# Performance work log

Hardware: AMD Instinct MI355X
Metric: run time of the kernel (lower is better)

Reference implementation:

```python
import jax, jax.numpy as jnp
import numpy as np

H = 1024      # hidden_size
I = 4096      # intermediate_size (4*H SwiGLU)
E = 8         # num_experts
TOPK = 2      # num_experts_per_tok


def setup_inputs() -> dict:
    key = jax.random.key(0)
    ks = jax.random.split(key, 6)
    B, S = 4, 2048
    hidden_states = jax.random.normal(ks[0], (B, S, H), dtype=jnp.float32)
    # router gate (no bias)
    gate_w = jax.random.normal(ks[1], (H, E), dtype=jnp.float32) * (1.0 / np.sqrt(H))
    # per-expert SwiGLU weights (xavier-ish scale)
    W1 = jax.random.normal(ks[2], (E, H, I), dtype=jnp.float32) * np.sqrt(2.0 / (H + I))
    W3 = jax.random.normal(ks[3], (E, H, I), dtype=jnp.float32) * np.sqrt(2.0 / (H + I))
    W2 = jax.random.normal(ks[4], (E, I, H), dtype=jnp.float32) * np.sqrt(2.0 / (H + I))
    # per-expert domain embedding (added to expert input), init std 0.02
    dom = jax.random.normal(ks[5], (E, H), dtype=jnp.float32) * 0.02
    return {"hidden_states": hidden_states, "gate_w": gate_w,
            "W1": W1, "W2": W2, "W3": W3, "dom": dom}


def reference(hidden_states, gate_w, W1, W2, W3, dom):
    B, S, Hd = hidden_states.shape
    x = hidden_states.reshape(-1, Hd)                      # [T, H]
    router_logits = x @ gate_w                             # [T, E]
    top_logits, top_idx = jax.lax.top_k(router_logits, TOPK)
    weights = jax.nn.softmax(top_logits, axis=-1)          # [T, K]
    # dense per-(token, expert) combine weight; 0 for unselected experts
    w_dense = jnp.einsum('tk,tke->te', weights,
                         jax.nn.one_hot(top_idx, E, dtype=weights.dtype))  # [T, E]
    out = jnp.zeros_like(x)
    for e in range(E):  # small fixed expert loop (structurally distinct weights)
        xe = x + dom[e]                                    # domain embedding add
        h = jax.nn.silu(xe @ W1[e]) * (xe @ W3[e])         # SwiGLU [T, I]
        out = out + w_dense[:, e:e + 1] * (h @ W2[e])      # weighted combine
    return out.reshape(B, S, Hd)
```

## Files before the change

kernel.cpp:

```cpp
#include <hip/hip_runtime.h>
#include <hip/hip_bf16.h>
#include <stdint.h>

#define T_TOK 8192
#define H_DIM 1024
#define I_DIM 4096
#define NEXP  8
#define BM    128
#define FBK   64
#define RT_TILES 136
#define RMAX (RT_TILES * BM)

typedef __attribute__((ext_vector_type(8))) short bf16x8;
typedef __attribute__((ext_vector_type(4))) float f32x4;

__device__ __forceinline__ unsigned short f2bf(float f) {
    unsigned int u = __float_as_uint(f);
    return (unsigned short)((u + 0x7FFFu + ((u >> 16) & 1u)) >> 16);
}
__device__ __forceinline__ unsigned int pk2(float a, float b) {
    return (unsigned int)f2bf(a) | ((unsigned int)f2bf(b) << 16);
}
__device__ __forceinline__ void gl_lds16(const void* g, void* l) {
    __builtin_amdgcn_global_load_lds(
        (const __attribute__((address_space(1))) unsigned int*)g,
        (__attribute__((address_space(3))) unsigned int*)l, 16, 0, 0);
}

__global__ __launch_bounds__(256) void router_k(const float* __restrict__ x,
                                                const float* __restrict__ gw,
                                                int2* __restrict__ ridx,
                                                float2* __restrict__ rw) {
    __shared__ float gwT[NEXP][H_DIM + 8];
    for (int i = threadIdx.x; i < H_DIM * NEXP; i += 256) {
        const int k = i >> 3, e = i & 7;
        gwT[e][k] = gw[i];
    }
    __syncthreads();
    const int wid = threadIdx.x >> 6, lane = threadIdx.x & 63;
    const int t = blockIdx.x * 4 + wid;
    const float4* xr = (const float4*)(x + (size_t)t * H_DIM);
    float acc[NEXP];
#pragma unroll
    for (int e = 0; e < NEXP; ++e) acc[e] = 0.f;
#pragma unroll
    for (int jj = 0; jj < 4; ++jj) {
        const float4 v = xr[jj * 64 + lane];
        const int kb = jj * 256 + lane * 4;
#pragma unroll
        for (int e = 0; e < NEXP; ++e) {
            const float4 g = *(const float4*)&gwT[e][kb];
            acc[e] += v.x * g.x + v.y * g.y + v.z * g.z + v.w * g.w;
        }
    }
#pragma unroll
    for (int e = 0; e < NEXP; ++e) {
#pragma unroll
        for (int off = 32; off > 0; off >>= 1) acc[e] += __shfl_xor(acc[e], off, 64);
    }
    if (lane == 0) {
        int i0 = 0; float l0 = acc[0];
#pragma unroll
        for (int e = 1; e < NEXP; ++e) if (acc[e] > l0) { l0 = acc[e]; i0 = e; }
        int i1 = -1; float l1 = -3.4e38f;
#pragma unroll
        for (int e = 0; e < NEXP; ++e) if (e != i0 && acc[e] > l1) { l1 = acc[e]; i1 = e; }
        float ee = __expf(l1 - l0);
        float w0 = 1.f / (1.f + ee);
        float w1 = 1.f - w0;
        ridx[t] = make_int2(i0, i1);
        rw[t]   = make_float2(w0, w1);
    }
}

__global__ __launch_bounds__(256) void plan_k(const int2* __restrict__ ridx,
                                              int* __restrict__ offs,
                                              int* __restrict__ rpos) {
    __shared__ int cnt[256][NEXP];
    __shared__ int base_sh[256][NEXP];
    const int tid = threadIdx.x;
    const int t0 = tid * (T_TOK / 256);
    int c[NEXP];
#pragma unroll
    for (int e = 0; e < NEXP; ++e) c[e] = 0;
    for (int j = 0; j < T_TOK / 256; ++j) {
        const int2 ii = ridx[t0 + j];
#pragma unroll
        for (int e = 0; e < NEXP; ++e)
            c[e] += (ii.x == e ? 1 : 0) + (ii.y == e ? 1 : 0);
    }
#pragma unroll
    for (int e = 0; e < NEXP; ++e) cnt[tid][e] = c[e];
    __syncthreads();
    if (tid == 0) {
        int tot[NEXP];
#pragma unroll
        for (int e = 0; e < NEXP; ++e) tot[e] = 0;
        for (int i = 0; i < 256; ++i)
#pragma unroll
            for (int e = 0; e < NEXP; ++e) tot[e] += cnt[i][e];
        int run[NEXP];
        int o = 0;
#pragma unroll
        for (int e = 0; e < NEXP; ++e) {
            offs[e] = o; run[e] = o;
            o += (tot[e] + BM - 1) & ~(BM - 1);
        }
        offs[NEXP] = o;
        for (int i = 0; i < 256; ++i)
#pragma unroll
            for (int e = 0; e < NEXP; ++e) {
                base_sh[i][e] = run[e];
                run[e] += cnt[i][e];
            }
    }
    __syncthreads();
    int b[NEXP];
#pragma unroll
    for (int e = 0; e < NEXP; ++e) b[e] = base_sh[tid][e];
    for (int j = 0; j < T_TOK / 256; ++j) {
        const int2 ii = ridx[t0 + j];
        int r0 = 0, r1 = 0;
#pragma unroll
        for (int e = 0; e < NEXP; ++e) r0 += (ii.x == e ? b[e] : 0);
#pragma unroll
        for (int e = 0; e < NEXP; ++e) b[e] += (ii.x == e ? 1 : 0);
#pragma unroll
        for (int e = 0; e < NEXP; ++e) r1 += (ii.y == e ? b[e] : 0);
#pragma unroll
        for (int e = 0; e < NEXP; ++e) b[e] += (ii.y == e ? 1 : 0);
        rpos[2 * (t0 + j)]     = r0;
        rpos[2 * (t0 + j) + 1] = r1;
    }
}

__global__ __launch_bounds__(256) void scatter_w13t_k(
        const float* __restrict__ x, const float* __restrict__ dom,
        const int2* __restrict__ ridx, const float2* __restrict__ rw,
        const int* __restrict__ rpos, float* __restrict__ rwgt,
        unsigned short* __restrict__ xg,
        const float* __restrict__ W1, const float* __restrict__ W3,
        unsigned short* __restrict__ w13) {
    __shared__ float st[64 * 65];
    if (blockIdx.x < 2048) {
        const int wid = threadIdx.x >> 6, lane = threadIdx.x & 63;
        const int t = blockIdx.x * 4 + wid;
        const int2 ii = ridx[t];
        const float2 ww = rw[t];
        const int r0 = rpos[2 * t], r1 = rpos[2 * t + 1];
        if (lane == 0) {
            rwgt[r0] = ww.x;
            rwgt[r1] = ww.y;
        }
        const float4* xr = (const float4*)(x + (size_t)t * H_DIM);
        float4 xv[4];
#pragma unroll
        for (int jj = 0; jj < 4; ++jj) xv[jj] = xr[jj * 64 + lane];
#pragma unroll
        for (int s = 0; s < 2; ++s) {
            const int e = s ? ii.y : ii.x;
            const int rr = s ? r1 : r0;
            const float4* dr = (const float4*)(dom + (size_t)e * H_DIM);
            unsigned short* op = xg + (size_t)rr * H_DIM;
#pragma unroll
            for (int jj = 0; jj < 4; ++jj) {
                const float4 b = dr[jj * 64 + lane];
                const int kb = jj * 256 + lane * 4;
                *(uint2*)(op + kb) = make_uint2(pk2(xv[jj].x + b.x, xv[jj].y + b.y),
                                                pk2(xv[jj].z + b.z, xv[jj].w + b.w));
            }
        }
    } else {
        const int idx = blockIdx.x - 2048;
        const int nt = idx & 63;
        const int kt = (idx >> 6) & 15;
        const int z  = idx >> 10;
        const int e = z >> 1, sel = z & 1;
        const float* src = (sel ? W3 : W1) + (size_t)e * H_DIM * I_DIM;
        const int t = threadIdx.x;
        const int kr = t >> 2, c0 = (t & 3) << 4;
        const float* sp = src + (size_t)(kt * 64 + kr) * I_DIM + nt * 64 + c0;
#pragma unroll
        for (int j = 0; j < 4; ++j) {
            float4 v = *(const float4*)(sp + j * 4);
            st[kr * 65 + c0 + j*4 + 0] = v.x; st[kr * 65 + c0 + j*4 + 1] = v.y;
            st[kr * 65 + c0 + j*4 + 2] = v.z; st[kr * 65 + c0 + j*4 + 3] = v.w;
        }
        __syncthreads();
        const int nl = t >> 2, k0 = (t & 3) << 4;
        const int n = nt * 64 + nl;
        const size_t drow = (size_t)e * 8192 + (size_t)((n >> 4) << 5) + (sel << 4) + (n & 15);
        unsigned short* dp = w13 + drow * H_DIM + kt * 64 + k0;
        unsigned int pk[8];
#pragma unroll
        for (int j = 0; j < 8; ++j)
            pk[j] = pk2(st[(k0 + 2*j) * 65 + nl], st[(k0 + 2*j + 1) * 65 + nl]);
        *(uint4*)dp = make_uint4(pk[0], pk[1], pk[2], pk[3]);
        *(uint4*)(dp + 8) = make_uint4(pk[4], pk[5], pk[6], pk[7]);
    }
}

__global__ __launch_bounds__(256, 3) void gemm1_w2t_k(
        const unsigned short* __restrict__ xg,
        const unsigned short* __restrict__ w13,
        const int* __restrict__ offs,
        unsigned short* __restrict__ h,
        const float* __restrict__ W2,
        unsigned short* __restrict__ w2t) {
    __shared__ unsigned short smem[2 * BM * FBK];
    if (blockIdx.x < 8704) {
        unsigned short* As = smem;
        unsigned short* Bs = smem + BM * FBK;
        const int wg = blockIdx.x;
        const int bx = wg & 63, by = wg >> 6;
        const int r0 = by * BM;
        if (r0 >= offs[NEXP]) return;
        int e = 0;
#pragma unroll
        for (int i = 1; i < NEXP; ++i) if (offs[i] <= r0) e = i;

        const int t = threadIdx.x, wid = t >> 6, lane = t & 63;
        const int srow = wid * 8 + (lane >> 3);
        const int schunk = (lane & 7) ^ (lane >> 3);
        const unsigned short* Agp = xg + (size_t)(r0 + srow) * H_DIM + (schunk << 3);
        const unsigned short* Bgp = w13 + ((size_t)e * 8192 + bx * 128 + srow) * H_DIM + (schunk << 3);
        unsigned short* Al = As + wid * 512;
        unsigned short* Bl = Bs + wid * 512;

        const int fr = lane & 15, g = lane >> 4, h3 = lane & 7;
        const int wr = (wid >> 1) * 64, wc = (wid & 1) * 64;

        f32x4 acc[4][4];
#pragma unroll
        for (int m = 0; m < 4; ++m)
#pragma unroll
            for (int n = 0; n < 4; ++n) acc[m][n] = (f32x4){0.f, 0.f, 0.f, 0.f};

#pragma unroll 1
        for (int kt = 0; kt < H_DIM / FBK; ++kt) {
            __syncthreads();
#pragma unroll
            for (int i = 0; i < 4; ++i) {
                gl_lds16(Agp + kt * FBK + i * 32 * H_DIM, Al + i * 2048);
                gl_lds16(Bgp + kt * FBK + i * 32 * H_DIM, Bl + i * 2048);
            }
            __syncthreads();
#pragma unroll
            for (int s = 0; s < 2; ++s) {
                const int pc = (((s << 2) + g) ^ h3) << 3;
                bf16x8 a[4], b[4];
#pragma unroll
                for (int m = 0; m < 4; ++m)
                    a[m] = *(const bf16x8*)&As[(wr + m * 16 + fr) * FBK + pc];
#pragma unroll
                for (int n = 0; n < 4; ++n)
                    b[n] = *(const bf16x8*)&Bs[(wc + n * 16 + fr) * FBK + pc];
#pragma unroll
                for (int m = 0; m < 4; ++m)
#pragma unroll
                    for (int n = 0; n < 4; ++n)
                        acc[m][n] = __builtin_amdgcn_mfma_f32_16x16x32_bf16(a[m], b[n], acc[m][n], 0, 0, 0);
            }
        }
        const int colbase = bx * 64 + ((wc >> 5) << 4) + fr;
#pragma unroll
        for (int m = 0; m < 4; ++m) {
            const int rbase = r0 + wr + m * 16 + (g << 2);
#pragma unroll
            for (int q = 0; q < 4; ++q) {
                unsigned short* hp = h + (size_t)(rbase + q) * I_DIM;
#pragma unroll
                for (int p = 0; p < 2; ++p) {
                    float p1 = acc[m][2 * p][q], p3 = acc[m][2 * p + 1][q];
                    float sv = p1 / (1.f + __expf(-p1));
                    hp[colbase + p * 16] = f2bf(sv * p3);
                }
            }
        }
    } else {
        float* st = (float*)smem;
        const int idx = blockIdx.x - 8704;
        const int nt = idx & 15;
        const int kt = (idx >> 4) & 63;
        const int e  = idx >> 10;
        const float* src = W2 + (size_t)e * I_DIM * H_DIM;
        const int t = threadIdx.x;
        const int kr = t >> 2, c0 = (t & 3) << 4;
        const float* sp = src + (size_t)(kt * 64 + kr) * H_DIM + nt * 64 + c0;
#pragma unroll
        for (int j = 0; j < 4; ++j) {
            float4 v = *(const float4*)(sp + j * 4);
            st[kr * 65 + c0 + j*4 + 0] = v.x; st[kr * 65 + c0 + j*4 + 1] = v.y;
            st[kr * 65 + c0 + j*4 + 2] = v.z; st[kr * 65 + c0 + j*4 + 3] = v.w;
        }
        __syncthreads();
        const int nl = t >> 2, k0 = (t & 3) << 4;
        unsigned short* dp = w2t + ((size_t)e * 1024 + nt * 64 + nl) * I_DIM + kt * 64 + k0;
        unsigned int pk[8];
#pragma unroll
        for (int j = 0; j < 8; ++j)
            pk[j] = pk2(st[(k0 + 2*j) * 65 + nl], st[(k0 + 2*j + 1) * 65 + nl]);
        *(uint4*)dp = make_uint4(pk[0], pk[1], pk[2], pk[3]);
        *(uint4*)(dp + 8) = make_uint4(pk[4], pk[5], pk[6], pk[7]);
    }
}

__global__ __launch_bounds__(256, 3) void gemm2_full_k(
        const unsigned short* __restrict__ hbuf,
        const unsigned short* __restrict__ w2t,
        const int* __restrict__ offs,
        float* __restrict__ y) {
    __shared__ unsigned short As[BM * FBK];
    __shared__ unsigned short Bs[BM * FBK];
    const int bid = blockIdx.x;
    const int idx = bid >> 3;
    const int by = (bid & 7) * 17 + (idx >> 3);
    const int bx = idx & 7;
    const int r0 = by * BM;
    if (r0 >= offs[NEXP]) return;
    int e = 0;
#pragma unroll
    for (int i = 1; i < NEXP; ++i) if (offs[i] <= r0) e = i;

    const int t = threadIdx.x, wid = t >> 6, lane = t & 63;
    const int srow = wid * 8 + (lane >> 3);
    const int schunk = (lane & 7) ^ (lane >> 3);
    const unsigned short* Agp = hbuf + (size_t)(r0 + srow) * I_DIM + (schunk << 3);
    const unsigned short* Bgp = w2t + ((size_t)e * 1024 + bx * 128 + srow) * I_DIM + (schunk << 3);
    unsigned short* Al = &As[wid * 512];
    unsigned short* Bl = &Bs[wid * 512];

    const int fr = lane & 15, g = lane >> 4, h3 = lane & 7;
    const int wr = (wid >> 1) * 64, wc = (wid & 1) * 64;

    f32x4 acc[4][4];
#pragma unroll
    for (int m = 0; m < 4; ++m)
#pragma unroll
        for (int n = 0; n < 4; ++n) acc[m][n] = (f32x4){0.f, 0.f, 0.f, 0.f};

#pragma unroll 1
    for (int kt = 0; kt < I_DIM / FBK; ++kt) {
        __syncthreads();
#pragma unroll
        for (int i = 0; i < 4; ++i) {
            gl_lds16(Agp + kt * FBK + (size_t)i * 32 * I_DIM, Al + i * 2048);
            gl_lds16(Bgp + kt * FBK + (size_t)i * 32 * I_DIM, Bl + i * 2048);
        }
        __syncthreads();
#pragma unroll
        for (int s = 0; s < 2; ++s) {
            const int pc = (((s << 2) + g) ^ h3) << 3;
            bf16x8 a[4], b[4];
#pragma unroll
            for (int m = 0; m < 4; ++m)
                a[m] = *(const bf16x8*)&As[(wr + m * 16 + fr) * FBK + pc];
#pragma unroll
            for (int n = 0; n < 4; ++n)
                b[n] = *(const bf16x8*)&Bs[(wc + n * 16 + fr) * FBK + pc];
#pragma unroll
            for (int m = 0; m < 4; ++m)
#pragma unroll
                for (int n = 0; n < 4; ++n)
                    acc[m][n] = __builtin_amdgcn_mfma_f32_16x16x32_bf16(a[m], b[n], acc[m][n], 0, 0, 0);
        }
    }
#pragma unroll
    for (int m = 0; m < 4; ++m) {
#pragma unroll
        for (int q = 0; q < 4; ++q) {
            const int rr = r0 + wr + m * 16 + (g << 2) + q;
            float* yp = y + (size_t)rr * H_DIM + bx * 128 + wc + fr;
#pragma unroll
            for (int n = 0; n < 4; ++n) yp[n * 16] = acc[m][n][q];
        }
    }
}

__global__ __launch_bounds__(256) void combine_k(const float* __restrict__ y,
                                                 const int* __restrict__ rpos,
                                                 const float* __restrict__ rwgt,
                                                 float* __restrict__ out) {
    const int wid = threadIdx.x >> 6, lane = threadIdx.x & 63;
    const int t = blockIdx.x * 4 + wid;
    const int ra = rpos[2 * t], rb = rpos[2 * t + 1];
    const float wa = rwgt[ra], wb = rwgt[rb];
    const float4* pa = (const float4*)(y + (size_t)ra * H_DIM);
    const float4* pb = (const float4*)(y + (size_t)rb * H_DIM);
    float4* po = (float4*)(out + (size_t)t * H_DIM);
#pragma unroll
    for (int j = 0; j < 4; ++j) {
        const int i = lane + j * 64;
        float4 a = pa[i], b = pb[i];
        po[i] = make_float4(wa * a.x + wb * b.x, wa * a.y + wb * b.y,
                            wa * a.z + wb * b.z, wa * a.w + wb * b.w);
    }
}

#define WS_OFFS  0
#define WS_RIDX  256
#define WS_RW    (WS_RIDX + T_TOK * 8)
#define WS_RWGT  (WS_RW + T_TOK * 8)
#define WS_RPOS  (WS_RWGT + RMAX * 4)
#define WS_W13   266752
#define WS_XG    (WS_W13 + (size_t)134217728)
#define WS_W2T   (WS_XG + (size_t)RMAX * H_DIM * 2)
#define WS_H     (WS_W2T + (size_t)67108864)
#define WS_Y     WS_W13

extern "C" void kernel_launch(void* const* d_in, const int* in_sizes, int n_in,
                              void* d_out, int out_size, void* d_ws, size_t ws_size,
                              hipStream_t stream) {
    (void)in_sizes; (void)n_in; (void)ws_size; (void)out_size;
    const float* x   = (const float*)d_in[0];
    const float* gw  = (const float*)d_in[1];
    const float* W1  = (const float*)d_in[2];
    const float* W2  = (const float*)d_in[3];
    const float* W3  = (const float*)d_in[4];
    const float* dom = (const float*)d_in[5];
    float* out = (float*)d_out;

    char* ws = (char*)d_ws;
    int*    offs   = (int*)(ws + WS_OFFS);
    int2*   ridx   = (int2*)(ws + WS_RIDX);
    float2* rw     = (float2*)(ws + WS_RW);
    float*  rwgt   = (float*)(ws + WS_RWGT);
    int*    rpos   = (int*)(ws + WS_RPOS);
    unsigned short* w13 = (unsigned short*)(ws + WS_W13);
    unsigned short* xg  = (unsigned short*)(ws + WS_XG);
    unsigned short* w2t = (unsigned short*)(ws + WS_W2T);
    unsigned short* hb  = (unsigned short*)(ws + WS_H);
    float*          y   = (float*)(ws + WS_Y);

    router_k<<<T_TOK / 4, 256, 0, stream>>>(x, gw, ridx, rw);
    plan_k<<<1, 256, 0, stream>>>(ridx, offs, rpos);
    scatter_w13t_k<<<2048 + 16384, 256, 0, stream>>>(x, dom, ridx, rw, rpos, rwgt, xg,
                                                     W1, W3, w13);
    gemm1_w2t_k<<<8704 + 8192, 256, 0, stream>>>(xg, w13, offs, hb, W2, w2t);
    gemm2_full_k<<<1088, 256, 0, stream>>>(hb, w2t, offs, y);
    combine_k<<<T_TOK / 4, 256, 0, stream>>>(y, rpos, rwgt, out);
}
```

Measured before the change: 642.3 us.

## Replace gemm1 with 256x256 tiled 4-stage pipelined kernel and per-expert tile list

Moves the W2 transpose-to-bf16 blocks into the scatter kernel and replaces the 128x128 gemm1 with a 512-thread, 256x256-tile kernel. The new kernel uses a 4-buffer global_load_lds pipeline with explicit vmcnt waits, split barriers and s_setprio around the MFMA blocks. plan_k now emits a compact per-expert tile list so blocks skip padded tiles, with row clamping and masked stores for partial tiles. The aim is higher MFMA utilisation and more operand reuse in the dominant GEMM, at the cost of more registers (launch bounds 512,2), occupancy pressure and hand-tuned wait counts that must match the exact load schedule.

```diff
diff --git a/kernel.cpp b/kernel.cpp
--- a/kernel.cpp
+++ b/kernel.cpp
@@ -10,6 +10,7 @@
 #define FBK   64
 #define RT_TILES 136
 #define RMAX (RT_TILES * BM)
+#define NTILE_MAX 72
 
 typedef __attribute__((ext_vector_type(8))) short bf16x8;
 typedef __attribute__((ext_vector_type(4))) float f32x4;
@@ -75,7 +76,8 @@
 
 __global__ __launch_bounds__(256) void plan_k(const int2* __restrict__ ridx,
                                               int* __restrict__ offs,
-                                              int* __restrict__ rpos) {
+                                              int* __restrict__ rpos,
+                                              int* __restrict__ tinfo) {
     __shared__ int cnt[256][NEXP];
     __shared__ int base_sh[256][NEXP];
     const int tid = threadIdx.x;
@@ -113,6 +115,17 @@
                 base_sh[i][e] = run[e];
                 run[e] += cnt[i][e];
             }
+        int ntl = 0;
+        for (int e = 0; e < NEXP; ++e) {
+            const int oe = offs[e], on = offs[e + 1];
+            for (int r = oe; r < on; r += 256) {
+                tinfo[1 + ntl] = r;
+                tinfo[1 + NTILE_MAX + ntl] = e;
+                tinfo[1 + 2 * NTILE_MAX + ntl] = (r + 256 < on) ? r + 256 : on;
+                ++ntl;
+            }
+        }
+        tinfo[0] = ntl;
     }
     __syncthreads();
     int b[NEXP];
@@ -140,7 +153,9 @@
         const int* __restrict__ rpos, float* __restrict__ rwgt,
         unsigned short* __restrict__ xg,
         const float* __restrict__ W1, const float* __restrict__ W3,
-        unsigned short* __restrict__ w13) {
+        unsigned short* __restrict__ w13,
+        const float* __restrict__ W2,
+        unsigned short* __restrict__ w2t) {
     __shared__ float st[64 * 65];
     if (blockIdx.x < 2048) {
         const int wid = threadIdx.x >> 6, lane = threadIdx.x & 63;
@@ -170,7 +185,7 @@
                                                 pk2(xv[jj].z + b.z, xv[jj].w + b.w));
             }
         }
-    } else {
+    } else if (blockIdx.x < 18432) {
         const int idx = blockIdx.x - 2048;
         const int nt = idx & 63;
         const int kt = (idx >> 6) & 15;
@@ -197,89 +212,8 @@
             pk[j] = pk2(st[(k0 + 2*j) * 65 + nl], st[(k0 + 2*j + 1) * 65 + nl]);
         *(uint4*)dp = make_uint4(pk[0], pk[1], pk[2], pk[3]);
         *(uint4*)(dp + 8) = make_uint4(pk[4], pk[5], pk[6], pk[7]);
-    }
-}
-
-__global__ __launch_bounds__(256, 3) void gemm1_w2t_k(
-        const unsigned short* __restrict__ xg,
-        const unsigned short* __restrict__ w13,
-        const int* __restrict__ offs,
-        unsigned short* __restrict__ h,
-        const float* __restrict__ W2,
-        unsigned short* __restrict__ w2t) {
-    __shared__ unsigned short smem[2 * BM * FBK];
-    if (blockIdx.x < 8704) {
-        unsigned short* As = smem;
-        unsigned short* Bs = smem + BM * FBK;
-        const int wg = blockIdx.x;
-        const int bx = wg & 63, by = wg >> 6;
-        const int r0 = by * BM;
-        if (r0 >= offs[NEXP]) return;
-        int e = 0;
-#pragma unroll
-        for (int i = 1; i < NEXP; ++i) if (offs[i] <= r0) e = i;
-
-        const int t = threadIdx.x, wid = t >> 6, lane = t & 63;
-        const int srow = wid * 8 + (lane >> 3);
-        const int schunk = (lane & 7) ^ (lane >> 3);
-        const unsigned short* Agp = xg + (size_t)(r0 + srow) * H_DIM + (schunk << 3);
-        const unsigned short* Bgp = w13 + ((size_t)e * 8192 + bx * 128 + srow) * H_DIM + (schunk << 3);
-        unsigned short* Al = As + wid * 512;
-        unsigned short* Bl = Bs + wid * 512;
-
-        const int fr = lane & 15, g = lane >> 4, h3 = lane & 7;
-        const int wr = (wid >> 1) * 64, wc = (wid & 1) * 64;
-
-        f32x4 acc[4][4];
-#pragma unroll
-        for (int m = 0; m < 4; ++m)
-#pragma unroll
-            for (int n = 0; n < 4; ++n) acc[m][n] = (f32x4){0.f, 0.f, 0.f, 0.f};
-
-#pragma unroll 1
-        for (int kt = 0; kt < H_DIM / FBK; ++kt) {
-            __syncthreads();
-#pragma unroll
-            for (int i = 0; i < 4; ++i) {
-                gl_lds16(Agp + kt * FBK + i * 32 * H_DIM, Al + i * 2048);
-                gl_lds16(Bgp + kt * FBK + i * 32 * H_DIM, Bl + i * 2048);
-            }
-            __syncthreads();
-#pragma unroll
-            for (int s = 0; s < 2; ++s) {
-                const int pc = (((s << 2) + g) ^ h3) << 3;
-                bf16x8 a[4], b[4];
-#pragma unroll
-                for (int m = 0; m < 4; ++m)
-                    a[m] = *(const bf16x8*)&As[(wr + m * 16 + fr) * FBK + pc];
-#pragma unroll
-                for (int n = 0; n < 4; ++n)
-                    b[n] = *(const bf16x8*)&Bs[(wc + n * 16 + fr) * FBK + pc];
-#pragma unroll
-                for (int m = 0; m < 4; ++m)
-#pragma unroll
-                    for (int n = 0; n < 4; ++n)
-                        acc[m][n] = __builtin_amdgcn_mfma_f32_16x16x32_bf16(a[m], b[n], acc[m][n], 0, 0, 0);
-            }
-        }
-        const int colbase = bx * 64 + ((wc >> 5) << 4) + fr;
-#pragma unroll
-        for (int m = 0; m < 4; ++m) {
-            const int rbase = r0 + wr + m * 16 + (g << 2);
-#pragma unroll
-            for (int q = 0; q < 4; ++q) {
-                unsigned short* hp = h + (size_t)(rbase + q) * I_DIM;
-#pragma unroll
-                for (int p = 0; p < 2; ++p) {
-                    float p1 = acc[m][2 * p][q], p3 = acc[m][2 * p + 1][q];
-                    float sv = p1 / (1.f + __expf(-p1));
-                    hp[colbase + p * 16] = f2bf(sv * p3);
-                }
-            }
-        }
     } else {
-        float* st = (float*)smem;
-        const int idx = blockIdx.x - 8704;
+        const int idx = blockIdx.x - 18432;
         const int nt = idx & 15;
         const int kt = (idx >> 4) & 63;
         const int e  = idx >> 10;
@@ -302,6 +236,117 @@
             pk[j] = pk2(st[(k0 + 2*j) * 65 + nl], st[(k0 + 2*j + 1) * 65 + nl]);
         *(uint4*)dp = make_uint4(pk[0], pk[1], pk[2], pk[3]);
         *(uint4*)(dp + 8) = make_uint4(pk[4], pk[5], pk[6], pk[7]);
+    }
+}
+
+#define SBAR __builtin_amdgcn_s_barrier()
+
+#define STG_A(tt, bf) do { \
+    gl_lds16(pA0 + (size_t)(tt) * 32, dA0 + (bf) * 16384); \
+    gl_lds16(pA1 + (size_t)(tt) * 32, dA0 + (bf) * 16384 + 512); } while (0)
+#define STG_B(tt, bf) do { \
+    gl_lds16(pB0 + (size_t)(tt) * 32, dA0 + (bf) * 16384 + 8192); \
+    gl_lds16(pB1 + (size_t)(tt) * 32, dA0 + (bf) * 16384 + 8192 + 512); } while (0)
+#define LD_A(s_, bf) do { _Pragma("unroll") for (int m2 = 0; m2 < 4; ++m2) \
+    a[m2] = *(const bf16x8*)(Ard + (bf) * 16384 + ((s_) * 64 + m2 * 16) * 32); } while (0)
+#define LD_B(bf) do { _Pragma("unroll") for (int n = 0; n < 4; ++n) \
+    b[n] = *(const bf16x8*)(Brd + (bf) * 16384 + (n * 16) * 32); } while (0)
+#define MM(s_) do { __builtin_amdgcn_s_setprio(1); \
+    _Pragma("unroll") for (int m2 = 0; m2 < 4; ++m2) \
+    _Pragma("unroll") for (int n = 0; n < 4; ++n) \
+        acc[(s_) * 4 + m2][n] = __builtin_amdgcn_mfma_f32_16x16x32_bf16(a[m2], b[n], acc[(s_) * 4 + m2][n], 0, 0, 0); \
+    __builtin_amdgcn_s_setprio(0); } while (0)
+#define GROUP(gg, ST, WAITM) do { \
+    const int bufc = (gg) & 3; \
+    const int bufs = ((gg) + 3) & 3; \
+    LD_A(0, bufc); LD_B(bufc); \
+    if (ST) STG_A((gg) + 3, bufs); \
+    SBAR; \
+    MM(0); \
+    SBAR; \
+    LD_A(1, bufc); \
+    if (ST) STG_B((gg) + 3, bufs); \
+    WAITM; \
+    SBAR; \
+    MM(1); \
+    SBAR; \
+} while (0)
+
+__global__ __launch_bounds__(512, 2) void gemm1_8ph_k(
+        const unsigned short* __restrict__ xg,
+        const unsigned short* __restrict__ w13,
+        const int* __restrict__ tinfo,
+        unsigned short* __restrict__ hb) {
+    __shared__ unsigned short lds_[4][2][256][32];
+    const int by = blockIdx.x >> 5;
+    if (by >= tinfo[0]) return;
+    const int bx = blockIdx.x & 31;
+    const int r0   = tinfo[1 + by];
+    const int e    = tinfo[1 + NTILE_MAX + by];
+    const int rend = tinfo[1 + 2 * NTILE_MAX + by];
+
+    const int t = threadIdx.x;
+    const int wid = t >> 6, lane = t & 63;
+    const int wm = wid >> 2, wn = wid & 3;
+    const int fr = lane & 15, lg = lane >> 4;
+
+    const int srow0 = wid * 32 + (lane >> 2);
+    const int srow1 = srow0 + 16;
+    const int slot  = lane & 3;
+    const int cc0 = (slot ^ ((srow0 >> 1) & 3)) << 3;
+    const int cc1 = (slot ^ ((srow1 >> 1) & 3)) << 3;
+    int ra0 = r0 + srow0; if (ra0 > RMAX - 1) ra0 = RMAX - 1;
+    int ra1 = r0 + srow1; if (ra1 > RMAX - 1) ra1 = RMAX - 1;
+    const unsigned short* pA0 = xg + (size_t)ra0 * H_DIM + cc0;
+    const unsigned short* pA1 = xg + (size_t)ra1 * H_DIM + cc1;
+    const size_t brow = (size_t)e * 8192 + (size_t)bx * 256;
+    const unsigned short* pB0 = w13 + (brow + srow0) * H_DIM + cc0;
+    const unsigned short* pB1 = w13 + (brow + srow1) * H_DIM + cc1;
+    unsigned short* lb  = &lds_[0][0][0][0];
+    unsigned short* dA0 = lb + (size_t)(wid * 32) * 32;
+
+    const int pc = (lg ^ ((fr >> 1) & 3)) << 3;
+    const unsigned short* Ard = lb + (wm * 128 + fr) * 32 + pc;
+    const unsigned short* Brd = lb + 8192 + (wn * 64 + fr) * 32 + pc;
+
+    f32x4 acc[8][4];
+#pragma unroll
+    for (int m = 0; m < 8; ++m)
+#pragma unroll
+        for (int n = 0; n < 4; ++n) acc[m][n] = (f32x4){0.f, 0.f, 0.f, 0.f};
+    bf16x8 a[4], b[4];
+
+    STG_A(0, 0); STG_B(0, 0);
+    STG_A(1, 1); STG_B(1, 1);
+    STG_A(2, 2); STG_B(2, 2);
+    asm volatile("s_waitcnt vmcnt(8)" ::: "memory");
+    SBAR;
+
+#pragma unroll 1
+    for (int g0 = 0; g0 < 29; ++g0) {
+        GROUP(g0, 1, asm volatile("s_waitcnt vmcnt(8)" ::: "memory"));
+    }
+    GROUP(29, 0, asm volatile("s_waitcnt vmcnt(4)" ::: "memory"));
+    GROUP(30, 0, asm volatile("s_waitcnt vmcnt(0)" ::: "memory"));
+    GROUP(31, 0, (void)0);
+
+    const int rowbase = r0 + wm * 128 + (lg << 2);
+    const int colbase = bx * 128 + wn * 32 + fr;
+#pragma unroll
+    for (int m = 0; m < 8; ++m) {
+#pragma unroll
+        for (int q = 0; q < 4; ++q) {
+            const int r = rowbase + m * 16 + q;
+            if (r < rend) {
+                unsigned short* hp = hb + (size_t)r * I_DIM + colbase;
+#pragma unroll
+                for (int p = 0; p < 2; ++p) {
+                    float p1 = acc[m][2 * p][q], p3 = acc[m][2 * p + 1][q];
+                    float sv = p1 / (1.f + __expf(-p1));
+                    hp[p * 16] = f2bf(sv * p3);
+                }
+            }
+        }
     }
 }
 
@@ -350,19 +395,19 @@
         __syncthreads();
 #pragma unroll
         for (int s = 0; s < 2; ++s) {
-            const int pc = (((s << 2) + g) ^ h3) << 3;
-            bf16x8 a[4], b[4];
+            const int pcc = (((s << 2) + g) ^ h3) << 3;
+            bf16x8 av[4], bv[4];
 #pragma unroll
             for (int m = 0; m < 4; ++m)
-                a[m] = *(const bf16x8*)&As[(wr + m * 16 + fr) * FBK + pc];
+                av[m] = *(const bf16x8*)&As[(wr + m * 16 + fr) * FBK + pcc];
 #pragma unroll
             for (int n = 0; n < 4; ++n)
-                b[n] = *(const bf16x8*)&Bs[(wc + n * 16 + fr) * FBK + pc];
+                bv[n] = *(const bf16x8*)&Bs[(wc + n * 16 + fr) * FBK + pcc];
 #pragma unroll
             for (int m = 0; m < 4; ++m)
 #pragma unroll
                 for (int n = 0; n < 4; ++n)
-                    acc[m][n] = __builtin_amdgcn_mfma_f32_16x16x32_bf16(a[m], b[n], acc[m][n], 0, 0, 0);
+                    acc[m][n] = __builtin_amdgcn_mfma_f32_16x16x32_bf16(av[m], bv[n], acc[m][n], 0, 0, 0);
         }
     }
 #pragma unroll
@@ -398,11 +443,12 @@
 }
 
 #define WS_OFFS  0
-#define WS_RIDX  256
+#define WS_TILE  256
+#define WS_RIDX  1280
 #define WS_RW    (WS_RIDX + T_TOK * 8)
 #define WS_RWGT  (WS_RW + T_TOK * 8)
 #define WS_RPOS  (WS_RWGT + RMAX * 4)
-#define WS_W13   266752
+#define WS_W13   267520
 #define WS_XG    (WS_W13 + (size_t)134217728)
 #define WS_W2T   (WS_XG + (size_t)RMAX * H_DIM * 2)
 #define WS_H     (WS_W2T + (size_t)67108864)
@@ -422,6 +468,7 @@
 
     char* ws = (char*)d_ws;
     int*    offs   = (int*)(ws + WS_OFFS);
+    int*    tinfo  = (int*)(ws + WS_TILE);
     int2*   ridx   = (int2*)(ws + WS_RIDX);
     float2* rw     = (float2*)(ws + WS_RW);
     float*  rwgt   = (float*)(ws + WS_RWGT);
@@ -433,10 +480,10 @@
     float*          y   = (float*)(ws + WS_Y);
 
     router_k<<<T_TOK / 4, 256, 0, stream>>>(x, gw, ridx, rw);
-    plan_k<<<1, 256, 0, stream>>>(ridx, offs, rpos);
-    scatter_w13t_k<<<2048 + 16384, 256, 0, stream>>>(x, dom, ridx, rw, rpos, rwgt, xg,
-                                                     W1, W3, w13);
-    gemm1_w2t_k<<<8704 + 8192, 256, 0, stream>>>(xg, w13, offs, hb, W2, w2t);
+    plan_k<<<1, 256, 0, stream>>>(ridx, offs, rpos, tinfo);
+    scatter_w13t_k<<<2048 + 16384 + 8192, 256, 0, stream>>>(x, dom, ridx, rw, rpos, rwgt, xg,
+                                                            W1, W3, w13, W2, w2t);
+    gemm1_8ph_k<<<NTILE_MAX * 32, 512, 0, stream>>>(xg, w13, tinfo, hb);
     gemm2_full_k<<<1088, 256, 0, stream>>>(hb, w2t, offs, y);
     combine_k<<<T_TOK / 4, 256, 0, stream>>>(y, rpos, rwgt, out);
 }
```

After: 711.5 us. +10.8%, slower.

## Split gemm2 K dimension in two and parallelize plan_k prefix sums

Applied to the files above, without the earlier changes.

The down-projection GEMM is split into two K halves launched as separate blocks. Each half writes its own partial-sum buffer, and the combine kernel adds the two partials before applying the routing weights. This doubles the block count to better fill the GPU's compute units. The cost is an extra fp32 partial buffer written and read back in combine. Separately, the serial single-thread per-expert totals and base-offset scan in plan_k is spread across 8 threads.

```diff
diff --git a/kernel.cpp b/kernel.cpp
--- a/kernel.cpp
+++ b/kernel.cpp
@@ -78,6 +78,8 @@
                                               int* __restrict__ rpos) {
     __shared__ int cnt[256][NEXP];
     __shared__ int base_sh[256][NEXP];
+    __shared__ int tot_sh[NEXP];
+    __shared__ int offs_sh[NEXP + 1];
     const int tid = threadIdx.x;
     const int t0 = tid * (T_TOK / 256);
     int c[NEXP];
@@ -92,27 +94,28 @@
 #pragma unroll
     for (int e = 0; e < NEXP; ++e) cnt[tid][e] = c[e];
     __syncthreads();
+    if (tid < NEXP) {
+        int s = 0;
+        for (int i = 0; i < 256; ++i) s += cnt[i][tid];
+        tot_sh[tid] = s;
+    }
+    __syncthreads();
     if (tid == 0) {
-        int tot[NEXP];
-#pragma unroll
-        for (int e = 0; e < NEXP; ++e) tot[e] = 0;
-        for (int i = 0; i < 256; ++i)
-#pragma unroll
-            for (int e = 0; e < NEXP; ++e) tot[e] += cnt[i][e];
-        int run[NEXP];
         int o = 0;
 #pragma unroll
         for (int e = 0; e < NEXP; ++e) {
-            offs[e] = o; run[e] = o;
-            o += (tot[e] + BM - 1) & ~(BM - 1);
-        }
-        offs[NEXP] = o;
-        for (int i = 0; i < 256; ++i)
-#pragma unroll
-            for (int e = 0; e < NEXP; ++e) {
-                base_sh[i][e] = run[e];
-                run[e] += cnt[i][e];
-            }
+            offs_sh[e] = o; offs[e] = o;
+            o += (tot_sh[e] + BM - 1) & ~(BM - 1);
+        }
+        offs_sh[NEXP] = o; offs[NEXP] = o;
+    }
+    __syncthreads();
+    if (tid < NEXP) {
+        int run = offs_sh[tid];
+        for (int i = 0; i < 256; ++i) {
+            base_sh[i][tid] = run;
+            run += cnt[i][tid];
+        }
     }
     __syncthreads();
     int b[NEXP];
@@ -305,7 +308,7 @@
     }
 }
 
-__global__ __launch_bounds__(256, 3) void gemm2_full_k(
+__global__ __launch_bounds__(256, 3) void gemm2_ksplit_k(
         const unsigned short* __restrict__ hbuf,
         const unsigned short* __restrict__ w2t,
         const int* __restrict__ offs,
@@ -313,8 +316,10 @@
     __shared__ unsigned short As[BM * FBK];
     __shared__ unsigned short Bs[BM * FBK];
     const int bid = blockIdx.x;
-    const int idx = bid >> 3;
-    const int by = (bid & 7) * 17 + (idx >> 3);
+    const int ks = (bid >= 1088) ? 1 : 0;
+    const int sb = bid - ks * 1088;
+    const int idx = sb >> 3;
+    const int by = (sb & 7) * 17 + (idx >> 3);
     const int bx = idx & 7;
     const int r0 = by * BM;
     if (r0 >= offs[NEXP]) return;
@@ -339,8 +344,9 @@
 #pragma unroll
         for (int n = 0; n < 4; ++n) acc[m][n] = (f32x4){0.f, 0.f, 0.f, 0.f};
 
+    const int kt0 = ks * 32;
 #pragma unroll 1
-    for (int kt = 0; kt < I_DIM / FBK; ++kt) {
+    for (int kt = kt0; kt < kt0 + 32; ++kt) {
         __syncthreads();
 #pragma unroll
         for (int i = 0; i < 4; ++i) {
@@ -350,27 +356,28 @@
         __syncthreads();
 #pragma unroll
         for (int s = 0; s < 2; ++s) {
-            const int pc = (((s << 2) + g) ^ h3) << 3;
-            bf16x8 a[4], b[4];
+            const int pcc = (((s << 2) + g) ^ h3) << 3;
+            bf16x8 av[4], bv[4];
 #pragma unroll
             for (int m = 0; m < 4; ++m)
-                a[m] = *(const bf16x8*)&As[(wr + m * 16 + fr) * FBK + pc];
+                av[m] = *(const bf16x8*)&As[(wr + m * 16 + fr) * FBK + pcc];
 #pragma unroll
             for (int n = 0; n < 4; ++n)
-                b[n] = *(const bf16x8*)&Bs[(wc + n * 16 + fr) * FBK + pc];
+                bv[n] = *(const bf16x8*)&Bs[(wc + n * 16 + fr) * FBK + pcc];
 #pragma unroll
             for (int m = 0; m < 4; ++m)
 #pragma unroll
                 for (int n = 0; n < 4; ++n)
-                    acc[m][n] = __builtin_amdgcn_mfma_f32_16x16x32_bf16(a[m], b[n], acc[m][n], 0, 0, 0);
-        }
-    }
+                    acc[m][n] = __builtin_amdgcn_mfma_f32_16x16x32_bf16(av[m], bv[n], acc[m][n], 0, 0, 0);
+        }
+    }
+    float* yo = y + (size_t)ks * ((size_t)RMAX * H_DIM);
 #pragma unroll
     for (int m = 0; m < 4; ++m) {
 #pragma unroll
         for (int q = 0; q < 4; ++q) {
             const int rr = r0 + wr + m * 16 + (g << 2) + q;
-            float* yp = y + (size_t)rr * H_DIM + bx * 128 + wc + fr;
+            float* yp = yo + (size_t)rr * H_DIM + bx * 128 + wc + fr;
 #pragma unroll
             for (int n = 0; n < 4; ++n) yp[n * 16] = acc[m][n][q];
         }
@@ -381,19 +388,24 @@
                                                  const int* __restrict__ rpos,
                                                  const float* __restrict__ rwgt,
                                                  float* __restrict__ out) {
+    const float* y1 = y + (size_t)RMAX * H_DIM;
     const int wid = threadIdx.x >> 6, lane = threadIdx.x & 63;
     const int t = blockIdx.x * 4 + wid;
     const int ra = rpos[2 * t], rb = rpos[2 * t + 1];
     const float wa = rwgt[ra], wb = rwgt[rb];
-    const float4* pa = (const float4*)(y + (size_t)ra * H_DIM);
-    const float4* pb = (const float4*)(y + (size_t)rb * H_DIM);
+    const float4* pa0 = (const float4*)(y  + (size_t)ra * H_DIM);
+    const float4* pa1 = (const float4*)(y1 + (size_t)ra * H_DIM);
+    const float4* pb0 = (const float4*)(y  + (size_t)rb * H_DIM);
+    const float4* pb1 = (const float4*)(y1 + (size_t)rb * H_DIM);
     float4* po = (float4*)(out + (size_t)t * H_DIM);
 #pragma unroll
     for (int j = 0; j < 4; ++j) {
         const int i = lane + j * 64;
-        float4 a = pa[i], b = pb[i];
-        po[i] = make_float4(wa * a.x + wb * b.x, wa * a.y + wb * b.y,
-                            wa * a.z + wb * b.z, wa * a.w + wb * b.w);
+        float4 a0 = pa0[i], a1 = pa1[i], b0 = pb0[i], b1 = pb1[i];
+        po[i] = make_float4(wa * (a0.x + a1.x) + wb * (b0.x + b1.x),
+                            wa * (a0.y + a1.y) + wb * (b0.y + b1.y),
+                            wa * (a0.z + a1.z) + wb * (b0.z + b1.z),
+                            wa * (a0.w + a1.w) + wb * (b0.w + b1.w));
     }
 }
 
@@ -437,6 +449,6 @@
     scatter_w13t_k<<<2048 + 16384, 256, 0, stream>>>(x, dom, ridx, rw, rpos, rwgt, xg,
                                                      W1, W3, w13);
     gemm1_w2t_k<<<8704 + 8192, 256, 0, stream>>>(xg, w13, offs, hb, W2, w2t);
-    gemm2_full_k<<<1088, 256, 0, stream>>>(hb, w2t, offs, y);
+    gemm2_ksplit_k<<<2176, 256, 0, stream>>>(hb, w2t, offs, y);
     combine_k<<<T_TOK / 4, 256, 0, stream>>>(y, rpos, rwgt, out);
 }
```

Result: faster. 608.3 us (-5.3%).
